# Performance work log

Measured on AMD Instinct MI355X. Metric: run time of the kernel, lower is better.

## Reference

```python
import jax, jax.numpy as jnp
import numpy as np

B, N, DIM = 16, 3136, 512
HEADS, AGENT, WINDOW = 8, 49, 14


def setup_inputs() -> dict:
    key = jax.random.key(0)
    ks = jax.random.split(key, 14)
    s = 0.02
    return {
        "x": jax.random.normal(ks[0], (B, N, DIM), jnp.float32),
        "w_qkv": jax.random.normal(ks[1], (3 * DIM, DIM), jnp.float32) * 0.02,
        "w_proj": jax.random.normal(ks[2], (DIM, DIM), jnp.float32) * 0.02,
        "b_proj": jnp.zeros((DIM,), jnp.float32),
        "w_dwc": jax.random.normal(ks[3], (DIM, 1, 3, 3), jnp.float32) * 0.1,
        "b_dwc": jnp.zeros((DIM,), jnp.float32),
        "an_bias": jax.random.normal(ks[4], (HEADS, AGENT, 7, 7), jnp.float32) * s,
        "na_bias": jax.random.normal(ks[5], (HEADS, AGENT, 7, 7), jnp.float32) * s,
        "ah_bias": jax.random.normal(ks[6], (1, HEADS, AGENT, WINDOW, 1), jnp.float32) * s,
        "aw_bias": jax.random.normal(ks[7], (1, HEADS, AGENT, 1, WINDOW), jnp.float32) * s,
        "ha_bias": jax.random.normal(ks[8], (1, HEADS, WINDOW, 1, AGENT), jnp.float32) * s,
        "wa_bias": jax.random.normal(ks[9], (1, HEADS, 1, WINDOW, AGENT), jnp.float32) * s,
        "ca_bias": jax.random.normal(ks[10], (1, HEADS, 1, AGENT), jnp.float32) * s,
    }


def reference(x, w_qkv, w_proj, b_proj, w_dwc, b_dwc, an_bias, na_bias,
              ah_bias, aw_bias, ha_bias, wa_bias, ca_bias):
    b, n, c = x.shape
    h = w = int(np.sqrt(n))            # 56x56, static
    nh, hd = HEADS, c // HEADS
    scale = hd ** -0.5
    ww = WINDOW * WINDOW               # 196

    qkv = x @ w_qkv.T                  # (b, n, 3c)
    q, k, v = jnp.split(qkv, 3, axis=-1)

    # agent tokens: adaptive avg-pool q to (7, 7)  (exact block mean, 56/7=8)
    pool = int(AGENT ** 0.5)
    q_img = q.reshape(b, h, w, c).transpose(0, 3, 1, 2)  # (b, c, h, w)
    pooled = q_img.reshape(b, c, pool, h // pool, pool, w // pool).mean(axis=(3, 5))
    agent = pooled.reshape(b, c, AGENT).transpose(0, 2, 1)  # (b, 49, c)

    qh = q.reshape(b, n, nh, hd).transpose(0, 2, 1, 3)      # (b, H, n, d)
    kh = k.reshape(b, n, nh, hd).transpose(0, 2, 1, 3)
    vh = v.reshape(b, n, nh, hd).transpose(0, 2, 1, 3)
    ah = agent.reshape(b, AGENT, nh, hd).transpose(0, 2, 1, 3)  # (b, H, 49, d)

    # ---- stage 1: agent -> kv attention ----
    pb1 = jax.image.resize(an_bias, (nh, AGENT, WINDOW, WINDOW), 'bilinear')
    pb1 = pb1.reshape(1, nh, AGENT, ww)
    pb2 = (ah_bias + aw_bias).reshape(1, nh, AGENT, ww)
    pb = jnp.broadcast_to(pb1 + pb2, (b, nh, AGENT, ww))
    scores1 = jnp.einsum('bhad,bhnd->bhan', ah * scale, kh)     # (b, H, 49, n)
    pb_up = jax.image.resize(pb, scores1.shape, 'bilinear')     # 196 -> n along last dim
    attn1 = jax.nn.softmax(scores1 + pb_up, axis=-1)
    agent_v = jnp.einsum('bhan,bhnd->bhad', attn1, vh)          # (b, H, 49, d)

    # ---- stage 2: query -> agent attention ----
    ab1 = jax.image.resize(na_bias, (nh, AGENT, WINDOW, WINDOW), 'bilinear')
    ab1 = ab1.reshape(1, nh, AGENT, ww).transpose(0, 1, 3, 2)   # (1, H, 196, 49)
    ab2 = (ha_bias + wa_bias).reshape(1, nh, ww, AGENT)
    ab = jnp.broadcast_to(ab1 + ab2, (b, nh, ww, AGENT))
    ab = jnp.concatenate([jnp.broadcast_to(ca_bias, (b, nh, 1, AGENT)), ab], axis=-2)
    scores2 = jnp.einsum('bhnd,bhad->bhna', qh * scale, ah)     # (b, H, n, 49)
    ab_up = jax.image.resize(ab, scores2.shape, 'bilinear')     # 197 -> n along dim -2
    attn2 = jax.nn.softmax(scores2 + ab_up, axis=-1)
    out = jnp.einsum('bhna,bhad->bhnd', attn2, agent_v)
    out = out.transpose(0, 2, 1, 3).reshape(b, n, c)

    # ---- depthwise-conv residual on v ----
    v_img = vh.transpose(0, 2, 1, 3).reshape(b, h, w, c).transpose(0, 3, 1, 2)
    dwc = jax.lax.conv_general_dilated(
        v_img, w_dwc, (1, 1), 'SAME',
        dimension_numbers=('NCHW', 'OIHW', 'NCHW'), feature_group_count=c)
    dwc = dwc + b_dwc[None, :, None, None]
    out = out + dwc.transpose(0, 2, 3, 1).reshape(b, n, c)

    return out @ w_proj.T + b_proj
```

## Files before the change

### kernel.cpp

```cpp
#include <hip/hip_runtime.h>

typedef unsigned short u16;
typedef unsigned int   u32;
typedef unsigned long long u64;
typedef float  f32x4  __attribute__((ext_vector_type(4)));
typedef __bf16 bf16x8 __attribute__((ext_vector_type(8)));

#define DEV static __device__ __forceinline__

DEV float bf2f(u16 u){ union{float f;u32 i;}v; v.i=((u32)u)<<16; return v.f; }
DEV float bflo(u32 u){ union{float f;u32 i;}v; v.i=u<<16; return v.f; }
DEV float bfhi(u32 u){ union{float f;u32 i;}v; v.i=u&0xffff0000u; return v.f; }
DEV u16   f2bf(float f){ union{float f;u32 i;}v; v.f=f; return (u16)((v.i + 0x7fffu + ((v.i>>16)&1u))>>16); }

DEV void async16(const void* g, void* l){
  __builtin_amdgcn_global_load_lds((const __attribute__((address_space(1))) void*)g,
                                   (__attribute__((address_space(3))) void*)l, 16, 0, 0);
}

__global__ __launch_bounds__(256) void cast_bf16(const float* __restrict__ in,
                                                 u16* __restrict__ out, int n4)
{
  int i = blockIdx.x*256 + threadIdx.x;
  if (i >= n4) return;
  float4 v = ((const float4*)in)[i];
  ushort4 o;
  o.x = f2bf(v.x); o.y = f2bf(v.y); o.z = f2bf(v.z); o.w = f2bf(v.w);
  ((ushort4*)out)[i] = o;
}

__global__ __launch_bounds__(512, 2) void gemm256(
    const u16* __restrict__ A, const u16* __restrict__ W, int K, int mode,
    u16* __restrict__ oq, u16* __restrict__ okk, u16* __restrict__ ov,
    float* __restrict__ of, const float* __restrict__ bias)
{
  __shared__ __align__(16) u16 As[2*16384];
  __shared__ __align__(16) u16 Bs[2*16384];
  const int tid  = threadIdx.x;
  const int w = tid >> 6, lane = tid & 63;
  const int wm = w >> 2, wn = w & 3;
  const int r16 = lane & 15, q4 = lane >> 4;
  const int xr = r16 & 7;
  const size_t Abase = (size_t)blockIdx.x * 256 * K;
  const size_t Bbase = (size_t)blockIdx.y * 256 * K;
  const int NT = K >> 6;

#define STAGE(t, half, arr) do { \
    const u16* _src = (arr) ? (W + Bbase) : (A + Abase); \
    u16* _dst = ((arr) ? Bs : As) + (((t) & 1) * 16384 + (half) * 8192); \
    const int _k0 = (t) << 6; \
    _Pragma("unroll") \
    for (int _i = 0; _i < 2; _i++) { \
      int _s = _i*512 + tid; \
      int _row = _s >> 3; \
      int _c = (_s & 7) ^ (_row & 7); \
      async16(_src + (size_t)((half)*128 + _row) * K + _k0 + _c*8, (char*)_dst + (size_t)_s * 16); \
    } \
  } while(0)

#define READ_A(MI0) do { \
    _Pragma("unroll") \
    for (int _i = 0; _i < 4; _i++) { \
      int _row = wm*128 + ((MI0)+_i)*16 + r16; \
      _Pragma("unroll") \
      for (int _ks = 0; _ks < 2; _ks++) \
        af[_i][_ks] = *(const bf16x8*)&As[boff + _row*64 + (((_ks*4 + q4) ^ xr) * 8)]; \
    } \
  } while(0)

#define READ_B() do { \
    _Pragma("unroll") \
    for (int _j = 0; _j < 4; _j++) { \
      int _row = wn*64 + _j*16 + r16; \
      _Pragma("unroll") \
      for (int _ks = 0; _ks < 2; _ks++) \
        bfr[_j][_ks] = *(const bf16x8*)&Bs[boff + _row*64 + (((_ks*4 + q4) ^ xr) * 8)]; \
    } \
  } while(0)

#define MFMA_Q(MI0, NI0) do { \
    _Pragma("unroll") \
    for (int _ks = 0; _ks < 2; _ks++) \
      _Pragma("unroll") \
      for (int _i = 0; _i < 4; _i++) \
        _Pragma("unroll") \
        for (int _j = 0; _j < 2; _j++) \
          acc[(MI0)+_i][(NI0)+_j] = __builtin_amdgcn_mfma_f32_16x16x32_bf16( \
              bfr[(NI0)+_j][_ks], af[_i][_ks], acc[(MI0)+_i][(NI0)+_j], 0,0,0); \
  } while(0)

  f32x4 acc[8][4];
  #pragma unroll
  for (int i=0;i<8;i++)
    #pragma unroll
    for (int j=0;j<4;j++) acc[i][j] = (f32x4){0.f,0.f,0.f,0.f};
  bf16x8 af[4][2], bfr[4][2];

  STAGE(0,0,0); STAGE(0,1,0); STAGE(0,0,1); STAGE(0,1,1);
  STAGE(1,0,1); STAGE(1,0,0); STAGE(1,1,0);
  asm volatile("s_waitcnt vmcnt(6)" ::: "memory");
  __builtin_amdgcn_s_barrier();

  for (int T = 0; T < NT; ++T) {
    const int boff = (T & 1) * 16384;
    READ_A(0);
    READ_B();
    if (T+1 < NT) STAGE(T+1, 1, 1);
    __builtin_amdgcn_s_barrier();
    asm volatile("s_waitcnt lgkmcnt(0)" ::: "memory");
    __builtin_amdgcn_sched_barrier(0);
    __builtin_amdgcn_s_setprio(1);
    MFMA_Q(0, 0);
    __builtin_amdgcn_s_setprio(0);
    __builtin_amdgcn_s_barrier();
    __builtin_amdgcn_s_setprio(1);
    MFMA_Q(0, 2);
    __builtin_amdgcn_s_setprio(0);
    __builtin_amdgcn_s_barrier();
    READ_A(4);
    if (T+2 < NT) STAGE(T+2, 0, 1);
    __builtin_amdgcn_s_barrier();
    asm volatile("s_waitcnt lgkmcnt(0)" ::: "memory");
    __builtin_amdgcn_sched_barrier(0);
    __builtin_amdgcn_s_setprio(1);
    MFMA_Q(4, 0);
    __builtin_amdgcn_s_setprio(0);
    __builtin_amdgcn_s_barrier();
    if (T+2 < NT) { STAGE(T+2, 0, 0); STAGE(T+2, 1, 0); }
    __builtin_amdgcn_s_setprio(1);
    MFMA_Q(4, 2);
    __builtin_amdgcn_s_setprio(0);
    if (T+2 < NT)      asm volatile("s_waitcnt vmcnt(6)" ::: "memory");
    else if (T+1 < NT) asm volatile("s_waitcnt vmcnt(0)" ::: "memory");
    __builtin_amdgcn_s_barrier();
  }

#undef STAGE
#undef READ_A
#undef READ_B
#undef MFMA_Q

  const int m0  = blockIdx.x*256 + wm*128;
  const int n0g = blockIdx.y*256 + wn*64;
  if (mode == 0){
    int sel = blockIdx.y >> 1;
    u16* dst = sel==0 ? oq : (sel==1 ? okk : ov);
    #pragma unroll
    for (int i=0;i<8;i++){
      int token = m0 + i*16 + r16;
      #pragma unroll
      for (int j=0;j<4;j++){
        int col = (n0g + j*16 + q4*4) & 511;
        uint2 pk;
        pk.x = (u32)f2bf(acc[i][j][0]) | ((u32)f2bf(acc[i][j][1]) << 16);
        pk.y = (u32)f2bf(acc[i][j][2]) | ((u32)f2bf(acc[i][j][3]) << 16);
        *(uint2*)&dst[(size_t)token*512 + col] = pk;
      }
    }
  } else {
    #pragma unroll
    for (int j=0;j<4;j++){
      int nbase = n0g + j*16 + q4*4;
      float4 b4 = *(const float4*)&bias[nbase];
      #pragma unroll
      for (int i=0;i<8;i++){
        int token = m0 + i*16 + r16;
        float4 o4 = { acc[i][j][0]+b4.x, acc[i][j][1]+b4.y,
                      acc[i][j][2]+b4.z, acc[i][j][3]+b4.w };
        *(float4*)&of[(size_t)token*512 + nbase] = o4;
      }
    }
  }
}

__global__ __launch_bounds__(256) void pool_q(const u16* __restrict__ qb, u16* __restrict__ agentb)
{
  int idx = blockIdx.x*256 + threadIdx.x;
  int c = idx & 511;
  int ba = idx >> 9;
  int a = ba & 63, b = ba >> 6;
  if (a >= 49) { agentb[idx] = 0; return; }
  int ay = a / 7, ax = a % 7;
  const u16* base = qb + (size_t)b*3136*512 + c;
  float acc = 0.f;
  #pragma unroll
  for (int iy=0; iy<8; iy++){
    int rowoff = ((ay*8 + iy)*56 + ax*8) * 512;
    #pragma unroll
    for (int ix=0; ix<8; ix++) acc += bf2f(base[(size_t)rowoff + ix*512]);
  }
  agentb[idx] = f2bf(acc * 0.015625f);
}

DEV void lin1(float c, int S, int& i0, int& i1, float& w){
  if (c <= 0.f){ i0=0; i1=0; w=0.f; }
  else if (c >= (float)(S-1)){ i0=S-1; i1=S-1; w=0.f; }
  else { i0=(int)c; i1=i0+1; w=c-(float)i0; }
}
DEV float bilin7(const float* s, int Y, int X){
  int y0,y1,x0,x1; float wy,wx;
  lin1(0.5f*Y - 0.25f, 7, y0,y1,wy);
  lin1(0.5f*X - 0.25f, 7, x0,x1,wx);
  float v0 = s[y0*7+x0] + wx*(s[y0*7+x1]-s[y0*7+x0]);
  float v1 = s[y1*7+x0] + wx*(s[y1*7+x1]-s[y1*7+x0]);
  return v0 + wy*(v1 - v0);
}
__global__ __launch_bounds__(256) void bias_pre(
    const float* __restrict__ an_bias, const float* __restrict__ na_bias,
    const float* __restrict__ ah_bias, const float* __restrict__ aw_bias,
    const float* __restrict__ ha_bias, const float* __restrict__ wa_bias,
    const float* __restrict__ ca_bias, float* __restrict__ PB, float* __restrict__ AB)
{
  int idx = blockIdx.x*256 + threadIdx.x;
  if (idx < 8*49*196){
    int j = idx % 196; int ha = idx / 196; int a = ha % 49, h = ha / 49;
    int wy = j / 14, wx = j % 14;
    PB[idx] = bilin7(an_bias + (h*49+a)*49, wy, wx)
            + ah_bias[(h*49+a)*14 + wy] + aw_bias[(h*49+a)*14 + wx];
  }
  int idx2 = idx - 8*49*196;
  if (idx2 >= 0 && idx2 < 8*197*49){
    int a = idx2 % 49; int hr = idx2 / 49; int r = hr % 197, h = hr / 197;
    float v;
    if (r == 0) v = ca_bias[h*49 + a];
    else {
      int j = r - 1; int wy = j / 14, wx = j % 14;
      v = bilin7(na_bias + (h*49+a)*49, wy, wx)
        + ha_bias[(h*14+wy)*49 + a] + wa_bias[(h*14+wx)*49 + a];
    }
    AB[idx2] = v;
  }
}

__global__ __launch_bounds__(256) void bias_expand2(
    const float* __restrict__ PB, const float* __restrict__ AB,
    float* __restrict__ PBIT, float* __restrict__ ABI)
{
  int idx = blockIdx.x*256 + threadIdx.x;
  if (idx < 1605632) {
    int a = idx & 63; int t = idx >> 6; int n = t % 3136; int h = t / 3136;
    float val = -1e30f;
    if (a < 49) {
      const float* row = PB + (h*49 + a)*196;
      float c1 = (n + 0.5f)*0.0625f - 0.5f;
      if (c1 <= 0.f) val = row[0];
      else if (c1 >= 195.f) val = row[195];
      else { int j0 = (int)c1; float w = c1 - (float)j0; val = row[j0] + w*(row[j0+1]-row[j0]); }
    }
    PBIT[idx] = val;
  } else {
    int idx2 = idx - 1605632;
    if (idx2 >= 1605632) return;
    int a = idx2 & 63; int t = idx2 >> 6; int n = t % 3136; int h = t / 3136;
    float val = -1e30f;
    if (a < 49) {
      float c2 = (n + 0.5f)*(197.0f/3136.0f) - 0.5f;
      int r0; float w;
      if (c2 <= 0.f) { r0 = 0; w = 0.f; }
      else if (c2 >= 196.f) { r0 = 196; w = 0.f; }
      else { r0 = (int)c2; w = c2 - (float)r0; }
      int r1 = (r0 < 196) ? r0 + 1 : 196;
      float v0 = AB[(h*197 + r0)*49 + a];
      float v1 = AB[(h*197 + r1)*49 + a];
      val = v0 + w*(v1 - v0);
    }
    ABI[idx2] = val;
  }
}

__global__ __launch_bounds__(256) void stage1_mfma(
    const u16* __restrict__ kb, const u16* __restrict__ vb,
    const u16* __restrict__ agentb, const float* __restrict__ PBIT,
    float* __restrict__ pav, float* __restrict__ psum)
{
  int bh = blockIdx.x, chunk = blockIdx.y;
  int b = bh >> 3, h = bh & 7;
  int tid = threadIdx.x, lane = tid & 63, w = tid >> 6;
  int r16 = lane & 15, q4 = lane >> 4;
  __shared__ __align__(16) u16 kld[64*64];
  __shared__ __align__(16) u16 vt[64*68];
  __shared__ __align__(16) u16 scb[64*72];

  int agent = w*16 + r16;
  bf16x8 bah[2];
  {
    const u16* ap = agentb + ((size_t)(b*64 + agent))*512 + h*64 + q4*8;
    bah[0] = *(const bf16x8*)ap;
    bah[1] = *(const bf16x8*)(ap + 32);
  }
  f32x4 Oacc[4];
  #pragma unroll
  for (int nt = 0; nt < 4; nt++) Oacc[nt] = (f32x4){0.f,0.f,0.f,0.f};
  float ssum = 0.f;
  int n0 = chunk * 448;
  const u16* kbase = kb + ((size_t)b*3136)*512 + h*64;
  const u16* vbase = vb + ((size_t)b*3136)*512 + h*64;

  for (int it = 0; it < 7; it++) {
    int nt0 = n0 + it*64;
    __syncthreads();
    #pragma unroll
    for (int i = 0; i < 2; i++) {
      int L = w*128 + i*64 + lane;
      int row = L >> 3, colc = (L & 7) ^ (row & 7);
      async16(kbase + (size_t)(nt0 + row)*512 + colc*8, (char*)kld + (w*128 + i*64)*16);
    }
    uint4 va[2]; int vtok[2], vdc[2];
    #pragma unroll
    for (int i = 0; i < 2; i++) {
      int c = tid + i*256;
      vtok[i] = c >> 3; vdc[i] = (c & 7)*8;
      va[i] = *(const uint4*)(vbase + (size_t)(nt0 + vtok[i])*512 + vdc[i]);
    }
    #pragma unroll
    for (int i = 0; i < 2; i++) {
      u32 uu[4] = {va[i].x, va[i].y, va[i].z, va[i].w};
      #pragma unroll
      for (int e = 0; e < 4; e++) {
        vt[(vdc[i] + 2*e + 0)*68 + vtok[i]] = (u16)(uu[e] & 0xffffu);
        vt[(vdc[i] + 2*e + 1)*68 + vtok[i]] = (u16)(uu[e] >> 16);
      }
    }
    __syncthreads();
    f32x4 S[4];
    #pragma unroll
    for (int mt = 0; mt < 4; mt++) S[mt] = (f32x4){0.f,0.f,0.f,0.f};
    #pragma unroll
    for (int ks = 0; ks < 2; ks++)
      #pragma unroll
      for (int mt = 0; mt < 4; mt++) {
        int row = mt*16 + r16;
        int colc = (ks*4 + q4) ^ (row & 7);
        bf16x8 afr = *(const bf16x8*)&kld[row*64 + colc*8];
        S[mt] = __builtin_amdgcn_mfma_f32_16x16x32_bf16(afr, bah[ks], S[mt], 0,0,0);
      }
    #pragma unroll
    for (int mt = 0; mt < 4; mt++) {
      u64 pk = 0;
      #pragma unroll
      for (int r = 0; r < 4; r++) {
        int tokl = mt*16 + q4*4 + r;
        float bias = PBIT[((size_t)h*3136 + nt0 + tokl)*64 + agent];
        float e = __expf(0.125f*S[mt][r] + bias);
        ssum += e;
        pk |= ((u64)f2bf(e)) << (16*r);
      }
      *(u64*)&scb[agent*72 + mt*16 + q4*4] = pk;
    }
    #pragma unroll
    for (int ks = 0; ks < 2; ks++) {
      bf16x8 ap = *(const bf16x8*)&scb[agent*72 + ks*32 + q4*8];
      #pragma unroll
      for (int nt = 0; nt < 4; nt++) {
        union { bf16x8 v; uint2 u[2]; } bb;
        int dim = nt*16 + r16;
        bb.u[0] = *(const uint2*)&vt[dim*68 + ks*32 + q4*8];
        bb.u[1] = *(const uint2*)&vt[dim*68 + ks*32 + q4*8 + 4];
        Oacc[nt] = __builtin_amdgcn_mfma_f32_16x16x32_bf16(ap, bb.v, Oacc[nt], 0,0,0);
      }
    }
  }
  ssum += __shfl_xor(ssum, 16);
  ssum += __shfl_xor(ssum, 32);
  size_t pb = (size_t)chunk*128 + bh;
  #pragma unroll
  for (int nt = 0; nt < 4; nt++)
    #pragma unroll
    for (int r = 0; r < 4; r++)
      pav[(pb*64 + (w*16 + q4*4 + r))*64 + nt*16 + r16] = Oacc[nt][r];
  if (lane < 16) psum[pb*64 + w*16 + lane] = ssum;
}

__global__ __launch_bounds__(256) void reduce_agv(
    const float* __restrict__ pav, const float* __restrict__ psum, u16* __restrict__ avTg)
{
  int idx = blockIdx.x*256 + threadIdx.x;
  int d = idx & 63, a = (idx >> 6) & 63, bh = idx >> 12;
  float val = 0.f;
  if (a < 49) {
    float acc = 0.f, s = 0.f;
    #pragma unroll
    for (int c = 0; c < 7; c++) {
      acc += pav[(((size_t)c*128 + bh)*64 + a)*64 + d];
      s   += psum[((size_t)c*128 + bh)*64 + a];
    }
    val = acc / s;
  }
  avTg[((size_t)bh*64 + d)*72 + a] = f2bf(val);
}

__global__ __launch_bounds__(256) void stage2_mfma(
    const u16* __restrict__ qb, const u16* __restrict__ agentb,
    const u16* __restrict__ avTg, const float* __restrict__ ABI,
    u16* __restrict__ aout)
{
  int bh = blockIdx.x, chunk = blockIdx.y;
  int b = bh >> 3, h = bh & 7;
  int tid = threadIdx.x, lane = tid & 63, w = tid >> 6;
  int r16 = lane & 15, q4 = lane >> 4;
  __shared__ __align__(16) u16 avs[64*72];
  __shared__ __align__(16) u16 scb2[4*16*72];

  const u16* avsrc = avTg + (size_t)bh*4608;
  #pragma unroll
  for (int rr = 0; rr < 3; rr++) {
    int c = rr*256 + w*64 + lane;
    if (c < 576) async16(avsrc + c*8, (char*)avs + ((size_t)rr*256 + w*64)*16);
  }
  bf16x8 bah[4][2];
  #pragma unroll
  for (int nt = 0; nt < 4; nt++) {
    const u16* ap = agentb + ((size_t)(b*64 + nt*16 + r16))*512 + h*64 + q4*8;
    bah[nt][0] = *(const bf16x8*)ap;
    bah[nt][1] = *(const bf16x8*)(ap + 32);
  }
  __syncthreads();

  u16* scw = scb2 + w*16*72;
  for (int t = 0; t < 7; t++) {
    int tok0 = (chunk*28 + w*7 + t)*16;
    bf16x8 aq[2];
    {
      const u16* qp = qb + ((size_t)b*3136 + tok0 + r16)*512 + h*64 + q4*8;
      aq[0] = *(const bf16x8*)qp;
      aq[1] = *(const bf16x8*)(qp + 32);
    }
    f32x4 S[4];
    #pragma unroll
    for (int nt = 0; nt < 4; nt++) S[nt] = (f32x4){0.f,0.f,0.f,0.f};
    #pragma unroll
    for (int ks = 0; ks < 2; ks++)
      #pragma unroll
      for (int nt = 0; nt < 4; nt++)
        S[nt] = __builtin_amdgcn_mfma_f32_16x16x32_bf16(aq[ks], bah[nt][ks], S[nt], 0,0,0);
    float rs[4] = {0.f,0.f,0.f,0.f};
    #pragma unroll
    for (int nt = 0; nt < 4; nt++)
      #pragma unroll
      for (int r = 0; r < 4; r++) {
        int tokl = q4*4 + r;
        float bias = ABI[((size_t)h*3136 + tok0 + tokl)*64 + nt*16 + r16];
        float e = __expf(0.125f*S[nt][r] + bias);
        rs[r] += e;
        scw[tokl*72 + nt*16 + r16] = f2bf(e);
      }
    #pragma unroll
    for (int m = 1; m <= 8; m <<= 1)
      #pragma unroll
      for (int r = 0; r < 4; r++) rs[r] += __shfl_xor(rs[r], m);
    f32x4 O[4];
    #pragma unroll
    for (int nt = 0; nt < 4; nt++) O[nt] = (f32x4){0.f,0.f,0.f,0.f};
    #pragma unroll
    for (int ks = 0; ks < 2; ks++) {
      bf16x8 ap2 = *(const bf16x8*)&scw[r16*72 + ks*32 + q4*8];
      #pragma unroll
      for (int nt = 0; nt < 4; nt++) {
        bf16x8 bv = *(const bf16x8*)&avs[(nt*16 + r16)*72 + ks*32 + q4*8];
        O[nt] = __builtin_amdgcn_mfma_f32_16x16x32_bf16(ap2, bv, O[nt], 0,0,0);
      }
    }
    float inv[4];
    #pragma unroll
    for (int r = 0; r < 4; r++) inv[r] = 1.0f / rs[r];
    #pragma unroll
    for (int nt = 0; nt < 4; nt++)
      #pragma unroll
      for (int r = 0; r < 4; r++)
        aout[((size_t)b*3136 + tok0 + q4*4 + r)*512 + h*64 + nt*16 + r16] = f2bf(O[nt][r]*inv[r]);
  }
}

__global__ __launch_bounds__(256) void dwc_add2(
    const u16* __restrict__ vb, const float* __restrict__ w_dwc,
    const float* __restrict__ b_dwc, u16* __restrict__ io)
{
  int wave = (blockIdx.x << 2) + (threadIdx.x >> 6);
  int lane = threadIdx.x & 63;
  int c0 = lane * 8;

  float wt[9][8];
  {
    float tmp[72];
    const float4* wp = (const float4*)(w_dwc + c0*9);
    #pragma unroll
    for (int i = 0; i < 18; i++) {
      float4 v4 = wp[i];
      tmp[4*i] = v4.x; tmp[4*i+1] = v4.y; tmp[4*i+2] = v4.z; tmp[4*i+3] = v4.w;
    }
    #pragma unroll
    for (int j = 0; j < 8; j++)
      #pragma unroll
      for (int tp = 0; tp < 9; tp++) wt[tp][j] = tmp[j*9 + tp];
  }
  float bias[8];
  {
    const float4* bp = (const float4*)(b_dwc + c0);
    float4 a4 = bp[0], b4 = bp[1];
    bias[0]=a4.x; bias[1]=a4.y; bias[2]=a4.z; bias[3]=a4.w;
    bias[4]=b4.x; bias[5]=b4.y; bias[6]=b4.z; bias[7]=b4.w;
  }

  int t0 = wave * 16;
  int b = t0 / 3136;
  int n0 = t0 - b*3136;
  const u16* vbase = vb + ((size_t)b*3136)*512 + c0;

  for (int ti = 0; ti < 16; ti++) {
    int n = n0 + ti;
    int y = n / 56, x = n - y*56;
    size_t toff = ((size_t)b*3136 + n)*512 + c0;
    float acc[8];
    {
      uint4 uo = *(const uint4*)(io + toff);
      u32 uu[4] = {uo.x, uo.y, uo.z, uo.w};
      #pragma unroll
      for (int e = 0; e < 4; e++) {
        acc[2*e+0] = bflo(uu[e]) + bias[2*e+0];
        acc[2*e+1] = bfhi(uu[e]) + bias[2*e+1];
      }
    }
    #pragma unroll
    for (int dy = 0; dy < 3; dy++) {
      int yy = y + dy - 1;
      if (yy < 0 || yy > 55) continue;
      #pragma unroll
      for (int dx = 0; dx < 3; dx++) {
        int xx = x + dx - 1;
        if (xx < 0 || xx > 55) continue;
        uint4 uv = *(const uint4*)(vbase + ((size_t)(yy*56 + xx) << 9));
        u32 uu[4] = {uv.x, uv.y, uv.z, uv.w};
        const float* wr = wt[dy*3 + dx];
        #pragma unroll
        for (int e = 0; e < 4; e++) {
          acc[2*e+0] += bflo(uu[e]) * wr[2*e+0];
          acc[2*e+1] += bfhi(uu[e]) * wr[2*e+1];
        }
      }
    }
    uint4 pk;
    pk.x = (u32)f2bf(acc[0]) | ((u32)f2bf(acc[1]) << 16);
    pk.y = (u32)f2bf(acc[2]) | ((u32)f2bf(acc[3]) << 16);
    pk.z = (u32)f2bf(acc[4]) | ((u32)f2bf(acc[5]) << 16);
    pk.w = (u32)f2bf(acc[6]) | ((u32)f2bf(acc[7]) << 16);
    *(uint4*)(io + toff) = pk;
  }
}

extern "C" void kernel_launch(void* const* d_in, const int* in_sizes, int n_in,
                              void* d_out, int out_size, void* d_ws, size_t ws_size,
                              hipStream_t stream)
{
  const float* x       = (const float*)d_in[0];
  const float* w_qkv   = (const float*)d_in[1];
  const float* w_proj  = (const float*)d_in[2];
  const float* b_proj  = (const float*)d_in[3];
  const float* w_dwc   = (const float*)d_in[4];
  const float* b_dwc   = (const float*)d_in[5];
  const float* an_bias = (const float*)d_in[6];
  const float* na_bias = (const float*)d_in[7];
  const float* ah_bias = (const float*)d_in[8];
  const float* aw_bias = (const float*)d_in[9];
  const float* ha_bias = (const float*)d_in[10];
  const float* wa_bias = (const float*)d_in[11];
  const float* ca_bias = (const float*)d_in[12];

  if (ws_size < 210000000u) return;

  char* p = (char*)d_ws;
  u16* regA   = (u16*)p;  p += 51380224;
  u16* qb     = (u16*)p;  p += 51380224;
  u16* kb     = (u16*)p;  p += 51380224;
  u16* vb     = (u16*)p;  p += 51380224;
  u16* wqkvb  = (u16*)p;  p += 1572864;
  u16* wprojb = (u16*)p;  p += 524288;
  u16* agentb = (u16*)p;  p += 1048576;
  float* PB   = (float*)p; p += 307456;
  float* AB   = (float*)p; p += 309248;

  float* PBIT = (float*)((char*)regA);
  float* ABI  = (float*)((char*)regA + 6422528);
  float* pav  = (float*)((char*)regA + 12845056);
  float* psum = (float*)((char*)regA + 27525120);
  u16*   avTg = (u16*)  ((char*)regA + 27754496);
  u16*   aout = kb;

  cast_bf16<<<25088, 256, 0, stream>>>(x, regA, 6422528);
  cast_bf16<<<768,   256, 0, stream>>>(w_qkv, wqkvb, 196608);
  cast_bf16<<<256,   256, 0, stream>>>(w_proj, wprojb, 65536);

  gemm256<<<dim3(196,6), 512, 0, stream>>>(regA, wqkvb, 512, 0, qb, kb, vb, nullptr, nullptr);
  pool_q<<<2048, 256, 0, stream>>>(qb, agentb);
  bias_pre<<<602, 256, 0, stream>>>(an_bias, na_bias, ah_bias, aw_bias, ha_bias, wa_bias, ca_bias, PB, AB);
  bias_expand2<<<12544, 256, 0, stream>>>(PB, AB, PBIT, ABI);
  stage1_mfma<<<dim3(128,7), 256, 0, stream>>>(kb, vb, agentb, PBIT, pav, psum);
  reduce_agv<<<2048, 256, 0, stream>>>(pav, psum, avTg);
  stage2_mfma<<<dim3(128,7), 256, 0, stream>>>(qb, agentb, avTg, ABI, aout);
  dwc_add2<<<784, 256, 0, stream>>>(vb, w_dwc, b_dwc, aout);
  gemm256<<<dim3(196,2), 512, 0, stream>>>(aout, wprojb, 512, 1, nullptr, nullptr, nullptr,
                                           (float*)d_out, b_proj);
}
```

Measured before the change: 529.6 us.

## Remap GEMM blocks across XCDs, drop a mid-loop barrier, vectorize pool_q

The GEMM block index is remapped so that consecutive logical tiles are spread across the 8 XCDs (hw&7 chiplet striping). The aim is better L2 reuse of shared A/B tiles within each chiplet. One s_barrier/setprio pair between two MFMA quarter-blocks is removed, so the two MFMA groups issue back to back. pool_q now has each thread load 8 bf16 channels with a 16-byte load and uses 8x fewer blocks, replacing scalar 2-byte gathers. The remap assumes the grid size is divisible by 8 (1176 and 392 both are).

```diff
diff --git a/kernel.cpp b/kernel.cpp
--- a/kernel.cpp
+++ b/kernel.cpp
@@ -41,8 +41,17 @@
   const int wm = w >> 2, wn = w & 3;
   const int r16 = lane & 15, q4 = lane >> 4;
   const int xr = r16 & 7;
-  const size_t Abase = (size_t)blockIdx.x * 256 * K;
-  const size_t Bbase = (size_t)blockIdx.y * 256 * K;
+
+  const int ny  = gridDim.y;
+  const int nwg = (int)gridDim.x * ny;
+  const int cpx = nwg >> 3;
+  const int hw  = blockIdx.x + gridDim.x*blockIdx.y;
+  const int lb  = (hw & 7)*cpx + (hw >> 3);
+  const int tx  = lb / ny;
+  const int ty  = lb - tx*ny;
+
+  const size_t Abase = (size_t)tx * 256 * K;
+  const size_t Bbase = (size_t)ty * 256 * K;
   const int NT = K >> 6;
 
 #define STAGE(t, half, arr) do { \
@@ -111,9 +120,6 @@
     __builtin_amdgcn_sched_barrier(0);
     __builtin_amdgcn_s_setprio(1);
     MFMA_Q(0, 0);
-    __builtin_amdgcn_s_setprio(0);
-    __builtin_amdgcn_s_barrier();
-    __builtin_amdgcn_s_setprio(1);
     MFMA_Q(0, 2);
     __builtin_amdgcn_s_setprio(0);
     __builtin_amdgcn_s_barrier();
@@ -140,10 +146,10 @@
 #undef READ_B
 #undef MFMA_Q
 
-  const int m0  = blockIdx.x*256 + wm*128;
-  const int n0g = blockIdx.y*256 + wn*64;
+  const int m0  = tx*256 + wm*128;
+  const int n0g = ty*256 + wn*64;
   if (mode == 0){
-    int sel = blockIdx.y >> 1;
+    int sel = ty >> 1;
     u16* dst = sel==0 ? oq : (sel==1 ? okk : ov);
     #pragma unroll
     for (int i=0;i<8;i++){
@@ -176,20 +182,30 @@
 __global__ __launch_bounds__(256) void pool_q(const u16* __restrict__ qb, u16* __restrict__ agentb)
 {
   int idx = blockIdx.x*256 + threadIdx.x;
-  int c = idx & 511;
-  int ba = idx >> 9;
+  int c8 = idx & 63;
+  int ba = idx >> 6;
   int a = ba & 63, b = ba >> 6;
-  if (a >= 49) { agentb[idx] = 0; return; }
+  u16* dst = agentb + ((size_t)(b*64 + a))*512 + c8*8;
+  if (a >= 49) { *(uint4*)dst = (uint4){0,0,0,0}; return; }
   int ay = a / 7, ax = a % 7;
-  const u16* base = qb + (size_t)b*3136*512 + c;
-  float acc = 0.f;
+  const u16* base = qb + ((size_t)b*3136 + (size_t)(ay*8)*56 + ax*8)*512 + c8*8;
+  float acc[8] = {0.f,0.f,0.f,0.f,0.f,0.f,0.f,0.f};
   #pragma unroll
   for (int iy=0; iy<8; iy++){
-    int rowoff = ((ay*8 + iy)*56 + ax*8) * 512;
-    #pragma unroll
-    for (int ix=0; ix<8; ix++) acc += bf2f(base[(size_t)rowoff + ix*512]);
-  }
-  agentb[idx] = f2bf(acc * 0.015625f);
+    #pragma unroll
+    for (int ix=0; ix<8; ix++){
+      uint4 uv = *(const uint4*)(base + ((size_t)(iy*56 + ix) << 9));
+      u32 uu[4] = {uv.x, uv.y, uv.z, uv.w};
+      #pragma unroll
+      for (int e=0;e<4;e++){ acc[2*e+0] += bflo(uu[e]); acc[2*e+1] += bfhi(uu[e]); }
+    }
+  }
+  uint4 pk;
+  pk.x = (u32)f2bf(acc[0]*0.015625f) | ((u32)f2bf(acc[1]*0.015625f) << 16);
+  pk.y = (u32)f2bf(acc[2]*0.015625f) | ((u32)f2bf(acc[3]*0.015625f) << 16);
+  pk.z = (u32)f2bf(acc[4]*0.015625f) | ((u32)f2bf(acc[5]*0.015625f) << 16);
+  pk.w = (u32)f2bf(acc[6]*0.015625f) | ((u32)f2bf(acc[7]*0.015625f) << 16);
+  *(uint4*)dst = pk;
 }
 
 DEV void lin1(float c, int S, int& i0, int& i1, float& w){
@@ -590,7 +606,7 @@
   cast_bf16<<<256,   256, 0, stream>>>(w_proj, wprojb, 65536);
 
   gemm256<<<dim3(196,6), 512, 0, stream>>>(regA, wqkvb, 512, 0, qb, kb, vb, nullptr, nullptr);
-  pool_q<<<2048, 256, 0, stream>>>(qb, agentb);
+  pool_q<<<256, 256, 0, stream>>>(qb, agentb);
   bias_pre<<<602, 256, 0, stream>>>(an_bias, na_bias, ah_bias, aw_bias, ha_bias, wa_bias, ca_bias, PB, AB);
   bias_expand2<<<12544, 256, 0, stream>>>(PB, AB, PBIT, ABI);
   stage1_mfma<<<dim3(128,7), 256, 0, stream>>>(kb, vb, agentb, PBIT, pav, psum);
```

Result: no change. 526.3 us (-0.6%).
